# Performance work log

Measured on AMD Instinct MI355X. Metric: run time of the kernel, lower is better.

Reference implementation:

```python
import jax, jax.numpy as jnp
import numpy as np

D = 768
N_HEADS = 12
HEAD_DIM = 64
INNER = N_HEADS * HEAD_DIM
SCALE = HEAD_DIM ** -0.5
EPS = 1e-5


def setup_inputs() -> dict:
    key = jax.random.key(0)
    ks = jax.random.split(key, 7)
    s = 0.02
    return {
        "x": jax.random.normal(ks[0], (2, 2048, D), dtype=jnp.float32),
        "Wq": jax.random.normal(ks[1], (D, INNER), dtype=jnp.float32) * s,
        "Wk": jax.random.normal(ks[2], (D, INNER), dtype=jnp.float32) * s,
        "Wv": jax.random.normal(ks[3], (D, INNER), dtype=jnp.float32) * s,
        "Wo": jax.random.normal(ks[4], (INNER, D), dtype=jnp.float32) * s,
        "bo": jnp.zeros((D,), dtype=jnp.float32),
        "gamma": jnp.ones((D,), dtype=jnp.float32),
        "beta": jnp.zeros((D,), dtype=jnp.float32),
    }


def _layernorm(x, gamma, beta):
    mu = jnp.mean(x, axis=-1, keepdims=True)
    var = jnp.var(x, axis=-1, keepdims=True)
    return (x - mu) * jax.lax.rsqrt(var + EPS) * gamma + beta


def reference(x, Wq, Wk, Wv, Wo, bo, gamma, beta):
    b, n, _ = x.shape
    h = _layernorm(x, gamma, beta)
    # project and split heads: [b, n, inner] -> [b, h, n, d]
    def split(t):
        return t.reshape(b, n, N_HEADS, HEAD_DIM).transpose(0, 2, 1, 3)
    Q = split(h @ Wq)
    K = split(h @ Wk)
    V = split(h @ Wv)
    # NOTE: module applies softmax first, THEN multiplies probs by scale
    attn = jnp.einsum('bhid,bhjd->bhij', Q, K)
    attn = jax.nn.softmax(attn, axis=-1) * SCALE
    vals = jnp.einsum('bhij,bhjd->bhid', attn, V)
    vals = vals.transpose(0, 2, 1, 3).reshape(b, n, INNER)
    out = vals @ Wo + bo
    return x + out
```

## Files before the change

### kernel.cpp

```cpp
#include <hip/hip_runtime.h>
#include <stdint.h>

typedef __bf16 bf16;
typedef __bf16 bf16x8 __attribute__((ext_vector_type(8)));
typedef float  f32x4  __attribute__((ext_vector_type(4)));
typedef unsigned short u16x4 __attribute__((ext_vector_type(4)));
typedef unsigned int   u32x4v __attribute__((ext_vector_type(4)));

#define SEQ   2048
#define DM    768
#define NH    12
#define HD    64
#define ATT_SCALE 0.125f
#define LOG2E 1.44269504f
#define LN_EPS 1e-5f

__device__ __forceinline__ void gload16(const void* g, void* l) {
  __builtin_amdgcn_global_load_lds((const __attribute__((address_space(1))) void*)g,
                                   (__attribute__((address_space(3))) void*)l,
                                   16, 0, 0);
}

__global__ __launch_bounds__(256) void prep_kernel(
    const float* __restrict__ x, const float* __restrict__ gamma,
    const float* __restrict__ beta, bf16* __restrict__ h,
    const float* __restrict__ Wq, const float* __restrict__ Wk,
    const float* __restrict__ Wv, const float* __restrict__ Wo,
    bf16* __restrict__ Wqkvt, bf16* __restrict__ Wot)
{
  __shared__ float smem[32*33];
  int bid = blockIdx.x, t = threadIdx.x;
  if (bid < 4096) {
    const float* xr = x + (size_t)bid*DM;
    float v0 = xr[t], v1 = xr[t+256], v2 = xr[t+512];
    float s = v0+v1+v2;
    float q = v0*v0+v1*v1+v2*v2;
    #pragma unroll
    for (int m=32;m>=1;m>>=1){ s += __shfl_xor(s,m,64); q += __shfl_xor(q,m,64); }
    float* rs = smem; float* rq = smem+8;
    int w = t>>6;
    if ((t&63)==0){ rs[w]=s; rq[w]=q; }
    __syncthreads();
    float S = rs[0]+rs[1]+rs[2]+rs[3];
    float Q = rq[0]+rq[1]+rq[2]+rq[3];
    float mean = S*(1.0f/DM);
    float var  = Q*(1.0f/DM) - mean*mean;
    float rstd = rsqrtf(var + LN_EPS);
    bf16* hr = h + (size_t)bid*DM;
    hr[t]     = (bf16)((v0-mean)*rstd*gamma[t]     + beta[t]);
    hr[t+256] = (bf16)((v1-mean)*rstd*gamma[t+256] + beta[t+256]);
    hr[t+512] = (bf16)((v2-mean)*rstd*gamma[t+512] + beta[t+512]);
  } else {
    int tb = bid - 4096;
    int z = tb/576, rem = tb%576;
    int r0 = (rem/24)*32, c0 = (rem%24)*32;
    int tx = t&31, ty = t>>5;
    float (*tile)[33] = (float(*)[33])smem;
    const float* src = (z==0)?Wq:(z==1)?Wk:(z==2)?Wv:Wo;
    #pragma unroll
    for (int i=ty;i<32;i+=8) tile[i][tx] = src[(size_t)(r0+i)*DM + c0+tx];
    __syncthreads();
    bf16* dst = (z<3) ? (Wqkvt + (size_t)z*DM*DM) : Wot;
    #pragma unroll
    for (int i=ty;i<32;i+=8) dst[(size_t)(c0+i)*DM + r0+tx] = (bf16)tile[tx][i];
  }
}

template<int BM, int BN, int BK, int WM, int WN, int EPI>
__global__ __launch_bounds__(256) void gemm_bt(
    const bf16* __restrict__ A, const bf16* __restrict__ Bt, int K,
    bf16* __restrict__ qk, bf16* __restrict__ vt,
    float* __restrict__ out, const float* __restrict__ bo, const float* __restrict__ xres)
{
  constexpr int MF  = BM/(WM*16);
  constexpr int NF  = BN/(WN*16);
  constexpr int GL  = (BM+BN)*BK/2048;
  constexpr int RPI = 512/BK;
  constexpr int KKN = BK/32;
  __shared__ bf16 As[3][BM][BK];
  __shared__ bf16 Bs[3][BN][BK];
  int tid = threadIdx.x, w = tid>>6, la = tid&63;
  int bn = blockIdx.x, bm = blockIdx.y;
  int wm = w / WN, wn = w % WN;
  int g = la>>4, li = la&15;
  int sr = la / (BK/8);
  int sc = (la % (BK/8))*8;
  f32x4 acc[MF][NF] = {};
  const int KT = K/BK;

  auto stage = [&](int kt, int bb) {
    int k0 = kt*BK;
    #pragma unroll
    for (int i=0;i<BM/(RPI*4);i++){ int r0 = (i*4+w)*RPI;
      gload16(A + ((size_t)(bm*BM + r0 + sr))*K + k0 + sc, &As[bb][r0][0]); }
    #pragma unroll
    for (int i=0;i<BN/(RPI*4);i++){ int r0 = (i*4+w)*RPI;
      gload16(Bt + ((size_t)(bn*BN + r0 + sr))*K + k0 + sc, &Bs[bb][r0][0]); }
  };

  stage(0,0); stage(1,1);
  asm volatile("s_waitcnt vmcnt(%0)" :: "n"(GL) : "memory");
  __builtin_amdgcn_s_barrier();
  __builtin_amdgcn_sched_barrier(0);

  for (int kt=0; kt<KT; ++kt) {
    int bb = kt%3;
    if (kt+2 < KT) stage(kt+2, (kt+2)%3);
    #pragma unroll
    for (int kk=0;kk<KKN;kk++){
      bf16x8 af[MF], bfr[NF];
      #pragma unroll
      for (int i=0;i<MF;i++) af[i]  = *(const bf16x8*)&As[bb][wm*(BM/WM)+i*16+li][kk*32+g*8];
      #pragma unroll
      for (int j=0;j<NF;j++) bfr[j] = *(const bf16x8*)&Bs[bb][wn*(BN/WN)+j*16+li][kk*32+g*8];
      __builtin_amdgcn_s_setprio(1);
      #pragma unroll
      for (int i=0;i<MF;i++)
        #pragma unroll
        for (int j=0;j<NF;j++)
          acc[i][j] = __builtin_amdgcn_mfma_f32_16x16x32_bf16(af[i], bfr[j], acc[i][j], 0,0,0);
      __builtin_amdgcn_s_setprio(0);
    }
    if (kt+1 < KT) {
      if (kt+2 < KT) asm volatile("s_waitcnt vmcnt(%0)" :: "n"(GL) : "memory");
      else           asm volatile("s_waitcnt vmcnt(0)" ::: "memory");
      __builtin_amdgcn_s_barrier();
      __builtin_amdgcn_sched_barrier(0);
    }
  }

  #pragma unroll
  for (int i=0;i<MF;i++){
    int row0 = bm*BM + wm*(BM/WM) + i*16 + g*4;
    #pragma unroll
    for (int j=0;j<NF;j++){
      int col = bn*BN + wn*(BN/WN) + j*16 + li;
      if (EPI==0){
        if (col < 1536) {
          float qs = (col < 768) ? LOG2E : 1.0f;
          #pragma unroll
          for (int r=0;r<4;r++) qk[(size_t)(row0+r)*1536 + col] = (bf16)(acc[i][j][r]*qs);
        } else {
          int cv = col - 1536; int hh = cv>>6, dd = cv&63;
          int b_ = row0>>11,  n0 = row0&2047;
          u16x4 u;
          #pragma unroll
          for (int r=0;r<4;r++){ bf16 bv = (bf16)acc[i][j][r];
            u[r] = __builtin_bit_cast(unsigned short, bv); }
          *reinterpret_cast<u16x4*>(vt + ((size_t)((b_*NH+hh)*HD+dd))*SEQ + n0) = u;
        }
      } else {
        float bb2 = bo[col];
        #pragma unroll
        for (int r=0;r<4;r++){ size_t idx = (size_t)(row0+r)*DM + col;
          out[idx] = acc[i][j][r] + bb2 + xres[idx]; }
      }
    }
  }
}

__global__ __launch_bounds__(512) void attn_kernel(
    const bf16* __restrict__ QK, const bf16* __restrict__ Vt,
    bf16* __restrict__ vals)
{
  __shared__ bf16 Ks[2][2][64][64];
  __shared__ bf16 Vs[2][2][64][64];
  int tid=threadIdx.x, w=tid>>6, la=tid&63;
  int half = w>>2, wl = w&3;
  int id = blockIdx.x;
  int xcd = id & 7, idx = id >> 3;
  int bh  = xcd*3 + idx/32;
  int qt  = idx & 31;
  int b = bh/NH, hh = bh%NH;
  int g=la>>4, li=la&15;
  int lr=la>>3;
  int lx=li&7;
  int lcs=((la&7)^lr)*8;
  size_t qrow0=(size_t)b*SEQ + qt*64;
  int kv0 = half*1024;

  bf16x8 qf[2];
  {
    const bf16* qp = QK + (qrow0 + wl*16 + li)*1536 + hh*64;
    qf[0] = *(const bf16x8*)(qp + g*8);
    qf[1] = *(const bf16x8*)(qp + 32 + g*8);
  }

  const bf16* Kbase = QK + (size_t)b*SEQ*1536 + 768 + hh*64;
  const bf16* Vbase = Vt + (size_t)(b*NH+hh)*HD*SEQ;

  auto stage = [&](int tt, int bbuf) {
    int j0 = kv0 + tt*64;
    #pragma unroll
    for (int i=0;i<2;i++){ int c=i*4+wl;
      gload16(Kbase + (size_t)(j0 + c*8 + lr)*1536 + lcs, &Ks[half][bbuf][c*8][0]);
      gload16(Vbase + (size_t)(c*8 + lr)*SEQ + j0 + lcs,  &Vs[half][bbuf][c*8][0]); }
  };

  stage(0,0);
  asm volatile("s_waitcnt vmcnt(0)" ::: "memory");
  __builtin_amdgcn_s_barrier();
  __builtin_amdgcn_sched_barrier(0);

  f32x4 o[4] = {};
  float lp[4] = {0.f,0.f,0.f,0.f};

  for (int t=0;t<16;t++){
    int bb = t&1;
    if (t+1 < 16) stage(t+1, bb^1);
    f32x4 s[4] = {};
    #pragma unroll
    for (int kk=0;kk<2;kk++){
      bf16x8 kf[4];
      #pragma unroll
      for (int nf=0;nf<4;nf++){
        int row = nf*16+li;
        kf[nf] = *(const bf16x8*)((const char*)&Ks[half][bb][0][0] + row*128 + (((kk*4+g)^lx)<<4));
      }
      __builtin_amdgcn_s_setprio(1);
      #pragma unroll
      for (int nf=0;nf<4;nf++)
        s[nf] = __builtin_amdgcn_mfma_f32_16x16x32_bf16(kf[nf], qf[kk], s[nf], 0,0,0);
      __builtin_amdgcn_s_setprio(0);
    }
    float p[4][4];
    #pragma unroll
    for (int nf=0;nf<4;nf++){
      #pragma unroll
      for (int r=0;r<4;r++){
        p[nf][r] = __builtin_amdgcn_exp2f(s[nf][r]);
        lp[nf] += p[nf][r];
      }
    }
    bf16x8 pa[2];
    #pragma unroll
    for (int ks=0;ks<2;ks++){
      unsigned int c00,c01,c10,c11;
      asm("v_cvt_pk_bf16_f32 %0, %1, %2" : "=v"(c00) : "v"(p[2*ks  ][0]), "v"(p[2*ks  ][1]));
      asm("v_cvt_pk_bf16_f32 %0, %1, %2" : "=v"(c01) : "v"(p[2*ks  ][2]), "v"(p[2*ks  ][3]));
      asm("v_cvt_pk_bf16_f32 %0, %1, %2" : "=v"(c10) : "v"(p[2*ks+1][0]), "v"(p[2*ks+1][1]));
      asm("v_cvt_pk_bf16_f32 %0, %1, %2" : "=v"(c11) : "v"(p[2*ks+1][2]), "v"(p[2*ks+1][3]));
      asm("v_permlane32_swap_b32 %0, %1" : "+v"(c00), "+v"(c10));
      asm("v_permlane32_swap_b32 %0, %1" : "+v"(c01), "+v"(c11));
      asm("v_permlane16_swap_b32 %0, %1" : "+v"(c00), "+v"(c10));
      asm("v_permlane16_swap_b32 %0, %1" : "+v"(c01), "+v"(c11));
      u32x4v cc = {c00, c01, c10, c11};
      pa[ks] = __builtin_bit_cast(bf16x8, cc);
    }
    #pragma unroll
    for (int ks=0;ks<2;ks++){
      bf16x8 vb[4];
      #pragma unroll
      for (int df=0;df<4;df++){
        int row = df*16+li;
        vb[df] = *(const bf16x8*)((const char*)&Vs[half][bb][0][0] + row*128 + (((ks*4+g)^lx)<<4));
      }
      __builtin_amdgcn_s_setprio(1);
      #pragma unroll
      for (int df=0;df<4;df++)
        o[df] = __builtin_amdgcn_mfma_f32_16x16x32_bf16(vb[df], pa[ks], o[df], 0,0,0);
      __builtin_amdgcn_s_setprio(0);
    }
    if (t+1 < 16) {
      asm volatile("s_waitcnt vmcnt(0)" ::: "memory");
      __builtin_amdgcn_s_barrier();
      __builtin_amdgcn_sched_barrier(0);
    }
  }
  float lsum = lp[0]+lp[1]+lp[2]+lp[3];
  lsum += __shfl_xor(lsum, 16, 64);
  lsum += __shfl_xor(lsum, 32, 64);
  __syncthreads();
  float* om  = (float*)&Ks[0][0][0][0];
  float* lmf = (float*)&Vs[0][0][0][0];
  if (half==1){
    float* orow = om + (wl*16+li)*68;
    #pragma unroll
    for (int df=0;df<4;df++)
      *reinterpret_cast<f32x4*>(orow + df*16 + g*4) = o[df];
    if (g==0) lmf[wl*16+li] = lsum;
  }
  __syncthreads();
  if (half==0){
    const float* orow = om + (wl*16+li)*68;
    float ltot = lsum + lmf[wl*16+li];
    float fac = ATT_SCALE / ltot;
    bf16* vrow = vals + (qrow0 + wl*16 + li)*DM + hh*64;
    #pragma unroll
    for (int df=0;df<4;df++){
      f32x4 pv = *reinterpret_cast<const f32x4*>(orow + df*16 + g*4);
      u16x4 u;
      #pragma unroll
      for (int r=0;r<4;r++){
        bf16 bv = (bf16)((o[df][r] + pv[r]) * fac);
        u[r] = __builtin_bit_cast(unsigned short, bv);
      }
      *reinterpret_cast<u16x4*>(vrow + df*16 + g*4) = u;
    }
  }
}

extern "C" void kernel_launch(void* const* d_in, const int* in_sizes, int n_in,
                              void* d_out, int out_size, void* d_ws, size_t ws_size,
                              hipStream_t stream)
{
  const float* x     = (const float*)d_in[0];
  const float* Wq    = (const float*)d_in[1];
  const float* Wk    = (const float*)d_in[2];
  const float* Wv    = (const float*)d_in[3];
  const float* Wo    = (const float*)d_in[4];
  const float* bo    = (const float*)d_in[5];
  const float* gamma = (const float*)d_in[6];
  const float* beta  = (const float*)d_in[7];
  float* out = (float*)d_out;
  char* ws = (char*)d_ws;

  bf16* h     = (bf16*)(ws + 0);
  bf16* vals  = (bf16*)(ws + 0);
  bf16* Wqkvt = (bf16*)(ws + 6291456);
  bf16* Wot   = (bf16*)(ws + 9830400);
  bf16* QKb   = (bf16*)(ws + 11010048);
  bf16* Vt    = (bf16*)(ws + 23592960);
  (void)ws_size; (void)in_sizes; (void)n_in; (void)out_size;

  prep_kernel<<<dim3(6400), dim3(256), 0, stream>>>(
      x, gamma, beta, h, Wq, Wk, Wv, Wo, Wqkvt, Wot);
  gemm_bt<128,128,32,2,2,0><<<dim3(18,32), dim3(256), 0, stream>>>(
      h, Wqkvt, DM, QKb, Vt, nullptr, nullptr, nullptr);
  attn_kernel<<<dim3(768), dim3(512), 0, stream>>>(QKb, Vt, vals);
  gemm_bt<64,64,64,2,2,1><<<dim3(12,64), dim3(256), 0, stream>>>(
      vals, Wot, DM, nullptr, nullptr, out, bo, x);
}
```

Baseline: 102.6 us.

## Process 128 query rows per attention block to reuse K/V tiles

Each wave now handles two 16-row query sub-tiles instead of one, so every block covers 128 query rows and the grid is halved to 384 blocks. Each K/V tile staged into LDS is reused by twice as many MFMAs, which halves global K/V traffic and LDS reads per query row. The combine buffer is re-laid out with an XOR-swizzled 64-float row stride to fit 128 rows in the existing shared memory. In exchange, register use per thread roughly doubles for accumulators and 384 blocks may underfill the 256 CUs, lowering parallelism.

After: 100.1 us. 2.5% less time.

```diff
diff --git a/kernel.cpp b/kernel.cpp
--- a/kernel.cpp
+++ b/kernel.cpp
@@ -169,21 +169,22 @@
   int half = w>>2, wl = w&3;
   int id = blockIdx.x;
   int xcd = id & 7, idx = id >> 3;
-  int bh  = xcd*3 + idx/32;
-  int qt  = idx & 31;
+  int bh  = xcd*3 + idx/16;
+  int qt  = idx & 15;
   int b = bh/NH, hh = bh%NH;
   int g=la>>4, li=la&15;
   int lr=la>>3;
   int lx=li&7;
   int lcs=((la&7)^lr)*8;
-  size_t qrow0=(size_t)b*SEQ + qt*64;
+  size_t qrow0=(size_t)b*SEQ + qt*128;
   int kv0 = half*1024;
 
-  bf16x8 qf[2];
-  {
-    const bf16* qp = QK + (qrow0 + wl*16 + li)*1536 + hh*64;
-    qf[0] = *(const bf16x8*)(qp + g*8);
-    qf[1] = *(const bf16x8*)(qp + 32 + g*8);
+  bf16x8 qf[2][2];
+  #pragma unroll
+  for (int qh=0;qh<2;qh++){
+    const bf16* qp = QK + (qrow0 + wl*32 + qh*16 + li)*1536 + hh*64;
+    qf[0][qh] = *(const bf16x8*)(qp + g*8);
+    qf[1][qh] = *(const bf16x8*)(qp + 32 + g*8);
   }
 
   const bf16* Kbase = QK + (size_t)b*SEQ*1536 + 768 + hh*64;
@@ -202,13 +203,13 @@
   __builtin_amdgcn_s_barrier();
   __builtin_amdgcn_sched_barrier(0);
 
-  f32x4 o[4] = {};
-  float lp[4] = {0.f,0.f,0.f,0.f};
+  f32x4 o[2][4] = {};
+  float lp[2][2] = {};
 
   for (int t=0;t<16;t++){
     int bb = t&1;
     if (t+1 < 16) stage(t+1, bb^1);
-    f32x4 s[4] = {};
+    f32x4 s[2][4] = {};
     #pragma unroll
     for (int kk=0;kk<2;kk++){
       bf16x8 kf[4];
@@ -219,33 +220,37 @@
       }
       __builtin_amdgcn_s_setprio(1);
       #pragma unroll
+      for (int nf=0;nf<4;nf++){
+        s[0][nf] = __builtin_amdgcn_mfma_f32_16x16x32_bf16(kf[nf], qf[kk][0], s[0][nf], 0,0,0);
+        s[1][nf] = __builtin_amdgcn_mfma_f32_16x16x32_bf16(kf[nf], qf[kk][1], s[1][nf], 0,0,0);
+      }
+      __builtin_amdgcn_s_setprio(0);
+    }
+    bf16x8 pa[2][2];
+    #pragma unroll
+    for (int qh=0;qh<2;qh++){
+      float p[4][4];
+      #pragma unroll
       for (int nf=0;nf<4;nf++)
-        s[nf] = __builtin_amdgcn_mfma_f32_16x16x32_bf16(kf[nf], qf[kk], s[nf], 0,0,0);
-      __builtin_amdgcn_s_setprio(0);
-    }
-    float p[4][4];
-    #pragma unroll
-    for (int nf=0;nf<4;nf++){
-      #pragma unroll
-      for (int r=0;r<4;r++){
-        p[nf][r] = __builtin_amdgcn_exp2f(s[nf][r]);
-        lp[nf] += p[nf][r];
-      }
-    }
-    bf16x8 pa[2];
-    #pragma unroll
-    for (int ks=0;ks<2;ks++){
-      unsigned int c00,c01,c10,c11;
-      asm("v_cvt_pk_bf16_f32 %0, %1, %2" : "=v"(c00) : "v"(p[2*ks  ][0]), "v"(p[2*ks  ][1]));
-      asm("v_cvt_pk_bf16_f32 %0, %1, %2" : "=v"(c01) : "v"(p[2*ks  ][2]), "v"(p[2*ks  ][3]));
-      asm("v_cvt_pk_bf16_f32 %0, %1, %2" : "=v"(c10) : "v"(p[2*ks+1][0]), "v"(p[2*ks+1][1]));
-      asm("v_cvt_pk_bf16_f32 %0, %1, %2" : "=v"(c11) : "v"(p[2*ks+1][2]), "v"(p[2*ks+1][3]));
-      asm("v_permlane32_swap_b32 %0, %1" : "+v"(c00), "+v"(c10));
-      asm("v_permlane32_swap_b32 %0, %1" : "+v"(c01), "+v"(c11));
-      asm("v_permlane16_swap_b32 %0, %1" : "+v"(c00), "+v"(c10));
-      asm("v_permlane16_swap_b32 %0, %1" : "+v"(c01), "+v"(c11));
-      u32x4v cc = {c00, c01, c10, c11};
-      pa[ks] = __builtin_bit_cast(bf16x8, cc);
+        #pragma unroll
+        for (int r=0;r<4;r++){
+          p[nf][r] = __builtin_amdgcn_exp2f(s[qh][nf][r]);
+          lp[qh][nf&1] += p[nf][r];
+        }
+      #pragma unroll
+      for (int ks=0;ks<2;ks++){
+        unsigned int c00,c01,c10,c11;
+        asm("v_cvt_pk_bf16_f32 %0, %1, %2" : "=v"(c00) : "v"(p[2*ks  ][0]), "v"(p[2*ks  ][1]));
+        asm("v_cvt_pk_bf16_f32 %0, %1, %2" : "=v"(c01) : "v"(p[2*ks  ][2]), "v"(p[2*ks  ][3]));
+        asm("v_cvt_pk_bf16_f32 %0, %1, %2" : "=v"(c10) : "v"(p[2*ks+1][0]), "v"(p[2*ks+1][1]));
+        asm("v_cvt_pk_bf16_f32 %0, %1, %2" : "=v"(c11) : "v"(p[2*ks+1][2]), "v"(p[2*ks+1][3]));
+        asm("v_permlane32_swap_b32 %0, %1" : "+v"(c00), "+v"(c10));
+        asm("v_permlane32_swap_b32 %0, %1" : "+v"(c01), "+v"(c11));
+        asm("v_permlane16_swap_b32 %0, %1" : "+v"(c00), "+v"(c10));
+        asm("v_permlane16_swap_b32 %0, %1" : "+v"(c01), "+v"(c11));
+        u32x4v cc = {c00, c01, c10, c11};
+        pa[qh][ks] = __builtin_bit_cast(bf16x8, cc);
+      }
     }
     #pragma unroll
     for (int ks=0;ks<2;ks++){
@@ -257,8 +262,10 @@
       }
       __builtin_amdgcn_s_setprio(1);
       #pragma unroll
-      for (int df=0;df<4;df++)
-        o[df] = __builtin_amdgcn_mfma_f32_16x16x32_bf16(vb[df], pa[ks], o[df], 0,0,0);
+      for (int qh=0;qh<2;qh++)
+        #pragma unroll
+        for (int df=0;df<4;df++)
+          o[qh][df] = __builtin_amdgcn_mfma_f32_16x16x32_bf16(vb[df], pa[qh][ks], o[qh][df], 0,0,0);
       __builtin_amdgcn_s_setprio(0);
     }
     if (t+1 < 16) {
@@ -267,35 +274,51 @@
       __builtin_amdgcn_sched_barrier(0);
     }
   }
-  float lsum = lp[0]+lp[1]+lp[2]+lp[3];
-  lsum += __shfl_xor(lsum, 16, 64);
-  lsum += __shfl_xor(lsum, 32, 64);
+  float lsum[2];
+  #pragma unroll
+  for (int qh=0;qh<2;qh++){
+    float v = lp[qh][0] + lp[qh][1];
+    v += __shfl_xor(v, 16, 64);
+    v += __shfl_xor(v, 32, 64);
+    lsum[qh] = v;
+  }
   __syncthreads();
   float* om  = (float*)&Ks[0][0][0][0];
   float* lmf = (float*)&Vs[0][0][0][0];
   if (half==1){
-    float* orow = om + (wl*16+li)*68;
-    #pragma unroll
-    for (int df=0;df<4;df++)
-      *reinterpret_cast<f32x4*>(orow + df*16 + g*4) = o[df];
-    if (g==0) lmf[wl*16+li] = lsum;
+    #pragma unroll
+    for (int qh=0;qh<2;qh++){
+      int row = wl*32 + qh*16 + li;
+      float* orow = om + row*64;
+      #pragma unroll
+      for (int df=0;df<4;df++){
+        int slot = (df*4 + g) ^ (row & 15);
+        *reinterpret_cast<f32x4*>(orow + slot*4) = o[qh][df];
+      }
+      if (g==0) lmf[row] = lsum[qh];
+    }
   }
   __syncthreads();
   if (half==0){
-    const float* orow = om + (wl*16+li)*68;
-    float ltot = lsum + lmf[wl*16+li];
-    float fac = ATT_SCALE / ltot;
-    bf16* vrow = vals + (qrow0 + wl*16 + li)*DM + hh*64;
-    #pragma unroll
-    for (int df=0;df<4;df++){
-      f32x4 pv = *reinterpret_cast<const f32x4*>(orow + df*16 + g*4);
-      u16x4 u;
-      #pragma unroll
-      for (int r=0;r<4;r++){
-        bf16 bv = (bf16)((o[df][r] + pv[r]) * fac);
-        u[r] = __builtin_bit_cast(unsigned short, bv);
-      }
-      *reinterpret_cast<u16x4*>(vrow + df*16 + g*4) = u;
+    #pragma unroll
+    for (int qh=0;qh<2;qh++){
+      int row = wl*32 + qh*16 + li;
+      const float* orow = om + row*64;
+      float ltot = lsum[qh] + lmf[row];
+      float fac = ATT_SCALE / ltot;
+      bf16* vrow = vals + (qrow0 + row)*DM + hh*64;
+      #pragma unroll
+      for (int df=0;df<4;df++){
+        int slot = (df*4 + g) ^ (row & 15);
+        f32x4 pv = *reinterpret_cast<const f32x4*>(orow + slot*4);
+        u16x4 u;
+        #pragma unroll
+        for (int r=0;r<4;r++){
+          bf16 bv = (bf16)((o[qh][df][r] + pv[r]) * fac);
+          u[r] = __builtin_bit_cast(unsigned short, bv);
+        }
+        *reinterpret_cast<u16x4*>(vrow + df*16 + g*4) = u;
+      }
     }
   }
 }
@@ -327,7 +350,7 @@
       x, gamma, beta, h, Wq, Wk, Wv, Wo, Wqkvt, Wot);
   gemm_bt<128,128,32,2,2,0><<<dim3(18,32), dim3(256), 0, stream>>>(
       h, Wqkvt, DM, QKb, Vt, nullptr, nullptr, nullptr);
-  attn_kernel<<<dim3(768), dim3(512), 0, stream>>>(QKb, Vt, vals);
+  attn_kernel<<<dim3(384), dim3(512), 0, stream>>>(QKb, Vt, vals);
   gemm_bt<64,64,64,2,2,1><<<dim3(12,64), dim3(256), 0, stream>>>(
       vals, Wot, DM, nullptr, nullptr, out, bo, x);
 }
```
